# Kernel tuning notes

Measured on AMD Instinct MI355X. Metric: run time of the kernel, lower is better.

## Reference

```python
import jax, jax.numpy as jnp
import numpy as np


def setup_inputs() -> dict:
    key = jax.random.key(0)
    k0, k1 = jax.random.split(key)
    B, S, T = 32, 512, 128
    return {
        "crf_score_0": jax.random.normal(k0, (B, S + 1, T, T), dtype=jnp.float32),
        "crf_score_1": jax.random.normal(k1, (B, S + 1, T), dtype=jnp.float32),
        "sof": 126,
        "eof": 127,
    }


def reference(crf_score_0, crf_score_1, sof, eof):
    # crf_score_0: [B, S+1, T, T], crf_score_1: [B, S+1, T]
    # Initial scores (note: original multiplies, not adds, at step 0)
    forscores = crf_score_0[:, 0, sof, :] * crf_score_1[:, 0, :]  # [B, T]

    # Move seq axis first for scan: [S, B, T, T] and [S, B, T]
    c0 = jnp.moveaxis(crf_score_0[:, 1:], 0, 1)
    c1 = jnp.moveaxis(crf_score_1[:, 1:], 0, 1)

    def fwd_step(fs, xs):
        t0, t1 = xs  # [B, T, T], [B, T]
        # cur[b, i, j] = fs[b, i] + t1[b, j] + t0[b, i, j]
        cur = fs[:, :, None] + t1[:, None, :] + t0
        new_fs = jnp.max(cur, axis=1)            # [B, T]
        bp = jnp.argmax(cur, axis=1).astype(jnp.int32)  # [B, T]
        return new_fs, bp

    _, back_points = jax.lax.scan(fwd_step, forscores, (c0, c1))  # bps: [S, B, T]

    # Backtrack exactly as the original loop: pointer starts at bp[-1][:, eof],
    # then for idx = S-1 .. 0: pointer = bp[idx][b, pointer]; decode[:, idx] = pointer.
    ptr0 = back_points[-1][:, eof]  # [B]

    def bwd_step(ptr, bp_t):
        new = jnp.take_along_axis(bp_t, ptr[:, None], axis=1)[:, 0]
        return new, new

    _, dec = jax.lax.scan(bwd_step, ptr0, back_points, reverse=True)  # [S, B]
    return dec.T.astype(jnp.int32)  # [B, S] decoded label indices
```

## Files before the change

kernel.cpp:

```cpp
#include <hip/hip_runtime.h>


constexpr int S = 512;
constexpr int T = 128;

__global__ __launch_bounds__(1024, 1)
void viterbi_fused(const float* __restrict__ c0, const float* __restrict__ c1,
                   const int* __restrict__ sofp, const int* __restrict__ eofp,
                   int* __restrict__ out)
{
    __shared__ float fs[2][T];
    __shared__ float pmax[32][T];
    __shared__ int   parg[32][T];
    __shared__ unsigned char bp[S][T];

    const int b   = blockIdx.x;
    const int tid = (int)threadIdx.x;
    const int jq  = tid & 31;
    const int g   = tid >> 5;
    const int col = jq * 4;
    const int row = g * 4;

    const float* c0b = c0 + (size_t)b * (S + 1) * T * T;
    const float* c1b = c1 + (size_t)b * (S + 1) * T;

    if (tid < T) {
        const int sof = sofp[0];
        fs[0][tid] = c0b[(size_t)sof * T + tid] * c1b[tid];
    }
    __syncthreads();

    {
    }
    const float* t0p = c0b + (size_t)1 * T * T;
    const float* t1p = c1b + (size_t)1 * T;
    float4 a0 = *(const float4*)(t0p + (size_t)(row + 0) * T + col);
    float4 a1 = *(const float4*)(t0p + (size_t)(row + 1) * T + col);
    float4 a2 = *(const float4*)(t0p + (size_t)(row + 2) * T + col);
    float4 a3 = *(const float4*)(t0p + (size_t)(row + 3) * T + col);
    float4 tv = *(const float4*)(t1p + col);

    int p = 0;
    for (int s = 1; s <= S; ++s) {
        float4 b0 = make_float4(0.f,0.f,0.f,0.f), b1 = b0, b2 = b0, b3 = b0, bt = b0;
        if (s < S) {
            const float* n0 = c0b + (size_t)(s + 1) * T * T;
            const float* n1 = c1b + (size_t)(s + 1) * T;
            b0 = *(const float4*)(n0 + (size_t)(row + 0) * T + col);
            b1 = *(const float4*)(n0 + (size_t)(row + 1) * T + col);
            b2 = *(const float4*)(n0 + (size_t)(row + 2) * T + col);
            b3 = *(const float4*)(n0 + (size_t)(row + 3) * T + col);
            bt = *(const float4*)(n1 + col);
        }

        const float f0 = fs[p][row + 0];
        const float f1 = fs[p][row + 1];
        const float f2 = fs[p][row + 2];
        const float f3 = fs[p][row + 3];

        float bx, by, bz, bw; int ix, iy, iz, iw; float v;
        bx = (f0 + tv.x) + a0.x; ix = row;
        by = (f0 + tv.y) + a0.y; iy = row;
        bz = (f0 + tv.z) + a0.z; iz = row;
        bw = (f0 + tv.w) + a0.w; iw = row;

        v = (f1 + tv.x) + a1.x; if (v > bx) { bx = v; ix = row + 1; }
        v = (f1 + tv.y) + a1.y; if (v > by) { by = v; iy = row + 1; }
        v = (f1 + tv.z) + a1.z; if (v > bz) { bz = v; iz = row + 1; }
        v = (f1 + tv.w) + a1.w; if (v > bw) { bw = v; iw = row + 1; }

        v = (f2 + tv.x) + a2.x; if (v > bx) { bx = v; ix = row + 2; }
        v = (f2 + tv.y) + a2.y; if (v > by) { by = v; iy = row + 2; }
        v = (f2 + tv.z) + a2.z; if (v > bz) { bz = v; iz = row + 2; }
        v = (f2 + tv.w) + a2.w; if (v > bw) { bw = v; iw = row + 2; }

        v = (f3 + tv.x) + a3.x; if (v > bx) { bx = v; ix = row + 3; }
        v = (f3 + tv.y) + a3.y; if (v > by) { by = v; iy = row + 3; }
        v = (f3 + tv.z) + a3.z; if (v > bz) { bz = v; iz = row + 3; }
        v = (f3 + tv.w) + a3.w; if (v > bw) { bw = v; iw = row + 3; }

        *(float4*)&pmax[g][col] = make_float4(bx, by, bz, bw);
        *(int4*)  &parg[g][col] = make_int4(ix, iy, iz, iw);
        __syncthreads();

        if (tid < T) {
            float bb = pmax[0][tid];
            int   ii = parg[0][tid];
            #pragma unroll
            for (int gg = 1; gg < 32; ++gg) {
                float vv = pmax[gg][tid];
                if (vv > bb) { bb = vv; ii = parg[gg][tid]; }
            }
            fs[p ^ 1][tid] = bb;
            bp[s - 1][tid] = (unsigned char)ii;
        }
        __syncthreads();

        p ^= 1;
        a0 = b0; a1 = b1; a2 = b2; a3 = b3; tv = bt;
    }

    if (tid == 0) {
        const int eof = eofp[0];
        int ptr = bp[S - 1][eof];
        for (int idx = S - 1; idx >= 0; --idx) {
            ptr = bp[idx][ptr];
            out[(size_t)b * S + idx] = ptr;
        }
    }
}

extern "C" void kernel_launch(void* const* d_in, const int* in_sizes, int n_in,
                              void* d_out, int out_size, void* d_ws, size_t ws_size,
                              hipStream_t stream)
{
    const float* c0  = (const float*)d_in[0];
    const float* c1  = (const float*)d_in[1];
    const int*   sof = (const int*)d_in[2];
    const int*   eof = (const int*)d_in[3];
    int*         out = (int*)d_out;

    const int B = in_sizes[1] / ((S + 1) * T);
    viterbi_fused<<<dim3(B), dim3(1024), 0, stream>>>(c0, c1, sof, eof, out);
}
```

Measured before the change: 849.4 us.

## Split Viterbi forward across 8 blocks per batch with global flag exchange

```diff
diff --git a/kernel.cpp b/kernel.cpp
--- a/kernel.cpp
+++ b/kernel.cpp
@@ -1,25 +1,170 @@
 #include <hip/hip_runtime.h>
 
 
-constexpr int S = 512;
-constexpr int T = 128;
+constexpr int S   = 512;
+constexpr int T   = 128;
+constexpr int NSL = 8;
+constexpr int CW  = 16;
+
+using u64 = unsigned long long;
+using u32 = unsigned int;
+
+__device__ __forceinline__ void bar_lds() {
+    asm volatile("s_waitcnt lgkmcnt(0)" ::: "memory");
+    __builtin_amdgcn_s_barrier();
+}
+__device__ __forceinline__ u32 flipf(u32 u)   { return u ^ (0x80000000u | (u32)((int)u >> 31)); }
+__device__ __forceinline__ u32 unflipf(u32 y) { return y ^ (0x80000000u | ~(u32)((int)y >> 31)); }
+__device__ __forceinline__ u64 aload(const u64* p) {
+    return __hip_atomic_load(p, __ATOMIC_RELAXED, __HIP_MEMORY_SCOPE_AGENT);
+}
+__device__ __forceinline__ void astore(u64* p, u64 v) {
+    __hip_atomic_store(p, v, __ATOMIC_RELAXED, __HIP_MEMORY_SCOPE_AGENT);
+}
+
+#define GLDS(srcp, dstp) \
+    __builtin_amdgcn_global_load_lds( \
+        (const __attribute__((address_space(1))) void*)(srcp), \
+        (__attribute__((address_space(3))) void*)(dstp), 16, 0, 0)
+
+__global__ __launch_bounds__(256, 1)
+void viterbi_fwdj(const float* __restrict__ c0, const float* __restrict__ c1,
+                  const int* __restrict__ sofp,
+                  u64* __restrict__ pub,
+                  unsigned char* __restrict__ bp)
+{
+    __shared__ float fs_lds[T];
+    __shared__ float t0s[2][T * CW];
+    __shared__ u64   wpart[2][CW];
+
+    const int g    = blockIdx.x;
+    const int b    = g & 31;
+    const int k    = g >> 5;
+    const int tid  = (int)threadIdx.x;
+    const int lane = tid & 63;
+
+    const float* c0b = c0 + (size_t)b * (S + 1) * T * T;
+    const float* c1b = c1 + (size_t)b * (S + 1) * T;
+    u64* pubB = pub + (size_t)b * 2 * T;
+
+    const bool is_cmp = tid >= 128;
+    const int  ct  = tid - 128;
+    const int  j   = ct & 15;
+    const int  rb  = ct >> 4;
+    const int  wv2 = (tid >> 6) - 2;
+
+    auto STAGE = [&](int ss, int buf) {
+        const float* srcbase = c0b + (size_t)ss * T * T + (size_t)k * CW;
+        #pragma unroll
+        for (int it = 0; it < 4; ++it) {
+            const int q   = wv2 * 4 + it;
+            const int row = q * 16 + (lane >> 2);
+            const float* src = srcbase + (size_t)row * T + (lane & 3) * 4;
+            float* dst = &t0s[buf][q * 256];
+            GLDS(src, dst);
+        }
+    };
+
+    if (tid < T) fs_lds[tid] = c0b[(size_t)sofp[0] * T + tid] * c1b[tid];
+    float t1c = 0.f, t1n = 0.f;
+    if (is_cmp) {
+        STAGE(1, 1);
+        t1c = c1b[(size_t)1 * T + k * CW + j];
+    }
+    asm volatile("s_waitcnt vmcnt(0)" ::: "memory");
+    bar_lds();
+
+    for (int s = 1; s <= S; ++s) {
+        const int par = s & 1;
+
+        if (is_cmp) {
+            const float* tp = &t0s[par][0];
+            const int r0 = rb * 16;
+            u64 key;
+            {
+                float v = (fs_lds[r0] + t1c) + tp[r0 * CW + j];
+                key = ((u64)flipf(__float_as_uint(v)) << 32) | (u32)(255 - r0);
+            }
+            #pragma unroll
+            for (int r = 1; r < 16; ++r) {
+                const int row = r0 + r;
+                float v = (fs_lds[row] + t1c) + tp[row * CW + j];
+                u64 kk = ((u64)flipf(__float_as_uint(v)) << 32) | (u32)(255 - row);
+                if (kk > key) key = kk;
+            }
+            { u64 p = __shfl_xor(key, 16, 64); if (p > key) key = p; }
+            { u64 p = __shfl_xor(key, 32, 64); if (p > key) key = p; }
+            if ((ct & 63) < 16) wpart[wv2][j] = key;
+
+            if (s < S) {
+                STAGE(s + 1, par ^ 1);
+                t1n = c1b[(size_t)(s + 1) * T + k * CW + j];
+            }
+        }
+        bar_lds();
+
+        if (is_cmp && ct < 16) {
+            u64 kk = wpart[0][j];
+            u64 k1 = wpart[1][j];
+            if (k1 > kk) kk = k1;
+            const u32 vb = unflipf((u32)(kk >> 32));
+            const int ii = 255 - (int)(kk & 0xFFu);
+            astore(&pubB[(size_t)par * T + k * CW + j], ((u64)vb << 32) | (u32)s);
+            bp[((size_t)b * S + (s - 1)) * T + k * CW + j] = (unsigned char)ii;
+            fs_lds[k * CW + j] = __uint_as_float(vb);
+        }
+        if (!is_cmp && (tid >> 4) != k) {
+            const u64* p = &pubB[(size_t)par * T + tid];
+            u64 v;
+            do { v = aload(p); } while ((u32)v != (u32)s);
+            fs_lds[tid] = __uint_as_float((u32)(v >> 32));
+        }
+        if (is_cmp) asm volatile("s_waitcnt vmcnt(0)" ::: "memory");
+        bar_lds();
+
+        t1c = t1n;
+    }
+}
 
 __global__ __launch_bounds__(1024, 1)
-void viterbi_fused(const float* __restrict__ c0, const float* __restrict__ c1,
-                   const int* __restrict__ sofp, const int* __restrict__ eofp,
-                   int* __restrict__ out)
+void viterbi_bwd(const unsigned char* __restrict__ bp,
+                 const int* __restrict__ eofp, int* __restrict__ out)
+{
+    __shared__ unsigned char lbp[S][T];
+    const int b   = blockIdx.x;
+    const int tid = (int)threadIdx.x;
+
+    const uint4* s4 = (const uint4*)(bp + (size_t)b * S * T);
+    uint4* d4 = (uint4*)&lbp[0][0];
+    #pragma unroll
+    for (int it = 0; it < 4; ++it) d4[tid + it * 1024] = s4[tid + it * 1024];
+    __syncthreads();
+
+    if (tid == 0) {
+        int ptr = lbp[S - 1][eofp[0]];
+        for (int idx = S - 1; idx >= 0; --idx) {
+            ptr = lbp[idx][ptr];
+            out[(size_t)b * S + idx] = ptr;
+        }
+    }
+}
+
+__global__ __launch_bounds__(1024, 1)
+void viterbi_fused_fb(const float* __restrict__ c0, const float* __restrict__ c1,
+                      const int* __restrict__ sofp, const int* __restrict__ eofp,
+                      int* __restrict__ out)
 {
     __shared__ float fs[2][T];
     __shared__ float pmax[32][T];
     __shared__ int   parg[32][T];
-    __shared__ unsigned char bp[S][T];
+    __shared__ unsigned char bpl[S][T];
 
     const int b   = blockIdx.x;
     const int tid = (int)threadIdx.x;
     const int jq  = tid & 31;
-    const int g   = tid >> 5;
+    const int gg2 = tid >> 5;
     const int col = jq * 4;
-    const int row = g * 4;
+    const int row = gg2 * 4;
 
     const float* c0b = c0 + (size_t)b * (S + 1) * T * T;
     const float* c1b = c1 + (size_t)b * (S + 1) * T;
@@ -30,29 +175,24 @@
     }
     __syncthreads();
 
-    {
-    }
-    const float* t0p = c0b + (size_t)1 * T * T;
-    const float* t1p = c1b + (size_t)1 * T;
+    const float* t0p = c0b + (size_t)T * T;
     float4 a0 = *(const float4*)(t0p + (size_t)(row + 0) * T + col);
     float4 a1 = *(const float4*)(t0p + (size_t)(row + 1) * T + col);
     float4 a2 = *(const float4*)(t0p + (size_t)(row + 2) * T + col);
     float4 a3 = *(const float4*)(t0p + (size_t)(row + 3) * T + col);
-    float4 tv = *(const float4*)(t1p + col);
+    float4 tv = *(const float4*)(c1b + T + col);
 
     int p = 0;
     for (int s = 1; s <= S; ++s) {
         float4 b0 = make_float4(0.f,0.f,0.f,0.f), b1 = b0, b2 = b0, b3 = b0, bt = b0;
         if (s < S) {
             const float* n0 = c0b + (size_t)(s + 1) * T * T;
-            const float* n1 = c1b + (size_t)(s + 1) * T;
             b0 = *(const float4*)(n0 + (size_t)(row + 0) * T + col);
             b1 = *(const float4*)(n0 + (size_t)(row + 1) * T + col);
             b2 = *(const float4*)(n0 + (size_t)(row + 2) * T + col);
             b3 = *(const float4*)(n0 + (size_t)(row + 3) * T + col);
-            bt = *(const float4*)(n1 + col);
-        }
-
+            bt = *(const float4*)(c1b + (size_t)(s + 1) * T + col);
+        }
         const float f0 = fs[p][row + 0];
         const float f1 = fs[p][row + 1];
         const float f2 = fs[p][row + 2];
@@ -63,48 +203,44 @@
         by = (f0 + tv.y) + a0.y; iy = row;
         bz = (f0 + tv.z) + a0.z; iz = row;
         bw = (f0 + tv.w) + a0.w; iw = row;
-
         v = (f1 + tv.x) + a1.x; if (v > bx) { bx = v; ix = row + 1; }
         v = (f1 + tv.y) + a1.y; if (v > by) { by = v; iy = row + 1; }
         v = (f1 + tv.z) + a1.z; if (v > bz) { bz = v; iz = row + 1; }
         v = (f1 + tv.w) + a1.w; if (v > bw) { bw = v; iw = row + 1; }
-
         v = (f2 + tv.x) + a2.x; if (v > bx) { bx = v; ix = row + 2; }
         v = (f2 + tv.y) + a2.y; if (v > by) { by = v; iy = row + 2; }
         v = (f2 + tv.z) + a2.z; if (v > bz) { bz = v; iz = row + 2; }
         v = (f2 + tv.w) + a2.w; if (v > bw) { bw = v; iw = row + 2; }
-
         v = (f3 + tv.x) + a3.x; if (v > bx) { bx = v; ix = row + 3; }
         v = (f3 + tv.y) + a3.y; if (v > by) { by = v; iy = row + 3; }
         v = (f3 + tv.z) + a3.z; if (v > bz) { bz = v; iz = row + 3; }
         v = (f3 + tv.w) + a3.w; if (v > bw) { bw = v; iw = row + 3; }
 
-        *(float4*)&pmax[g][col] = make_float4(bx, by, bz, bw);
-        *(int4*)  &parg[g][col] = make_int4(ix, iy, iz, iw);
+        *(float4*)&pmax[gg2][col] = make_float4(bx, by, bz, bw);
+        *(int4*)  &parg[gg2][col] = make_int4(ix, iy, iz, iw);
         __syncthreads();
 
         if (tid < T) {
             float bb = pmax[0][tid];
             int   ii = parg[0][tid];
             #pragma unroll
-            for (int gg = 1; gg < 32; ++gg) {
-                float vv = pmax[gg][tid];
-                if (vv > bb) { bb = vv; ii = parg[gg][tid]; }
+            for (int qq2 = 1; qq2 < 32; ++qq2) {
+                float vv = pmax[qq2][tid];
+                if (vv > bb) { bb = vv; ii = parg[qq2][tid]; }
             }
             fs[p ^ 1][tid] = bb;
-            bp[s - 1][tid] = (unsigned char)ii;
+            bpl[s - 1][tid] = (unsigned char)ii;
         }
         __syncthreads();
-
         p ^= 1;
         a0 = b0; a1 = b1; a2 = b2; a3 = b3; tv = bt;
     }
 
     if (tid == 0) {
         const int eof = eofp[0];
-        int ptr = bp[S - 1][eof];
+        int ptr = bpl[S - 1][eof];
         for (int idx = S - 1; idx >= 0; --idx) {
-            ptr = bp[idx][ptr];
+            ptr = bpl[idx][ptr];
             out[(size_t)b * S + idx] = ptr;
         }
     }
@@ -121,5 +257,15 @@
     int*         out = (int*)d_out;
 
     const int B = in_sizes[1] / ((S + 1) * T);
-    viterbi_fused<<<dim3(B), dim3(1024), 0, stream>>>(c0, c1, sof, eof, out);
-}
+
+    const size_t pub_b = (size_t)B * 2 * T * 8;
+    const size_t bp_b  = (size_t)B * S * T;
+    if (B == 32 && ws_size >= pub_b + bp_b) {
+        u64* pubw = (u64*)d_ws;
+        unsigned char* bpw = (unsigned char*)d_ws + pub_b;
+        viterbi_fwdj<<<dim3(B * NSL), dim3(256), 0, stream>>>(c0, c1, sof, pubw, bpw);
+        viterbi_bwd<<<dim3(B), dim3(1024), 0, stream>>>(bpw, eof, out);
+    } else {
+        viterbi_fused_fb<<<dim3(B), dim3(1024), 0, stream>>>(c0, c1, sof, eof, out);
+    }
+}
```

After: 846.9 us. About the same (-0.3%).

## Reduce argmax with wave shuffles and one barrier per step, double-buffered register prefetch

Applied to the files above, without the earlier changes.

```diff
diff --git a/kernel.cpp b/kernel.cpp
--- a/kernel.cpp
+++ b/kernel.cpp
@@ -4,101 +4,111 @@
 constexpr int S = 512;
 constexpr int T = 128;
 
+using u64 = unsigned long long;
+using u32 = unsigned int;
+
+__device__ __forceinline__ void bar_lds() {
+    asm volatile("s_waitcnt lgkmcnt(0)" ::: "memory");
+    __builtin_amdgcn_s_barrier();
+}
+__device__ __forceinline__ u32 flipf(u32 u)   { return u ^ (0x80000000u | (u32)((int)u >> 31)); }
+__device__ __forceinline__ u32 unflipf(u32 y) { return y ^ (0x80000000u | ~(u32)((int)y >> 31)); }
+
 __global__ __launch_bounds__(1024, 1)
-void viterbi_fused(const float* __restrict__ c0, const float* __restrict__ c1,
-                   const int* __restrict__ sofp, const int* __restrict__ eofp,
-                   int* __restrict__ out)
+void viterbi_one(const float* __restrict__ c0, const float* __restrict__ c1,
+                 const int* __restrict__ sofp, const int* __restrict__ eofp,
+                 int* __restrict__ out)
 {
     __shared__ float fs[2][T];
-    __shared__ float pmax[32][T];
-    __shared__ int   parg[32][T];
     __shared__ unsigned char bp[S][T];
 
     const int b   = blockIdx.x;
     const int tid = (int)threadIdx.x;
-    const int jq  = tid & 31;
-    const int g   = tid >> 5;
-    const int col = jq * 4;
-    const int row = g * 4;
+    const int j   = tid >> 3;
+    const int ih  = tid & 7;
+    const int r0  = ih * 16;
 
     const float* c0b = c0 + (size_t)b * (S + 1) * T * T;
     const float* c1b = c1 + (size_t)b * (S + 1) * T;
 
-    if (tid < T) {
-        const int sof = sofp[0];
-        fs[0][tid] = c0b[(size_t)sof * T + tid] * c1b[tid];
+    if (tid < T) fs[0][tid] = c0b[(size_t)sofp[0] * T + tid] * c1b[tid];
+
+    const float* pA = c0b + (size_t)T * T + (size_t)r0 * T + j;
+    const float* pB = pA + T * T;
+    float tA = c1b[(size_t)1 * T + j];
+    float tB = c1b[(size_t)2 * T + j];
+
+#define LOAD16(P, ptr)                                                        \
+    P##0  = (ptr)[0 * T];  P##1  = (ptr)[1 * T];  P##2  = (ptr)[2 * T];       \
+    P##3  = (ptr)[3 * T];  P##4  = (ptr)[4 * T];  P##5  = (ptr)[5 * T];       \
+    P##6  = (ptr)[6 * T];  P##7  = (ptr)[7 * T];  P##8  = (ptr)[8 * T];       \
+    P##9  = (ptr)[9 * T];  P##10 = (ptr)[10 * T]; P##11 = (ptr)[11 * T];      \
+    P##12 = (ptr)[12 * T]; P##13 = (ptr)[13 * T]; P##14 = (ptr)[14 * T];      \
+    P##15 = (ptr)[15 * T];
+
+    float A0, A1, A2, A3, A4, A5, A6, A7, A8, A9, A10, A11, A12, A13, A14, A15;
+    float B0, B1, B2, B3, B4, B5, B6, B7, B8, B9, B10, B11, B12, B13, B14, B15;
+    LOAD16(A, pA)
+    LOAD16(B, pB)
+
+    bar_lds();
+
+#define STEP(SS, P, tc)                                                       \
+    {                                                                         \
+        const int par = (SS) & 1;                                             \
+        const float* fsr = &fs[par ^ 1][r0];                                  \
+        float4 f0 = *(const float4*)(fsr);                                    \
+        float4 f1 = *(const float4*)(fsr + 4);                                \
+        float4 f2 = *(const float4*)(fsr + 8);                                \
+        float4 f3 = *(const float4*)(fsr + 12);                               \
+        float bv, v; int br;                                                  \
+        bv = (f0.x + tc) + P##0;  br = 0;                                     \
+        v = (f0.y + tc) + P##1;  if (v > bv) { bv = v; br = 1;  }             \
+        v = (f0.z + tc) + P##2;  if (v > bv) { bv = v; br = 2;  }             \
+        v = (f0.w + tc) + P##3;  if (v > bv) { bv = v; br = 3;  }             \
+        v = (f1.x + tc) + P##4;  if (v > bv) { bv = v; br = 4;  }             \
+        v = (f1.y + tc) + P##5;  if (v > bv) { bv = v; br = 5;  }             \
+        v = (f1.z + tc) + P##6;  if (v > bv) { bv = v; br = 6;  }             \
+        v = (f1.w + tc) + P##7;  if (v > bv) { bv = v; br = 7;  }             \
+        v = (f2.x + tc) + P##8;  if (v > bv) { bv = v; br = 8;  }             \
+        v = (f2.y + tc) + P##9;  if (v > bv) { bv = v; br = 9;  }             \
+        v = (f2.z + tc) + P##10; if (v > bv) { bv = v; br = 10; }             \
+        v = (f2.w + tc) + P##11; if (v > bv) { bv = v; br = 11; }             \
+        v = (f3.x + tc) + P##12; if (v > bv) { bv = v; br = 12; }             \
+        v = (f3.y + tc) + P##13; if (v > bv) { bv = v; br = 13; }             \
+        v = (f3.z + tc) + P##14; if (v > bv) { bv = v; br = 14; }             \
+        v = (f3.w + tc) + P##15; if (v > bv) { bv = v; br = 15; }             \
+        u64 key = ((u64)flipf(__float_as_uint(bv)) << 32)                     \
+                | (u32)(255 - (r0 + br));                                     \
+        { u64 p = __shfl_xor(key, 1, 64); if (p > key) key = p; }             \
+        { u64 p = __shfl_xor(key, 2, 64); if (p > key) key = p; }             \
+        { u64 p = __shfl_xor(key, 4, 64); if (p > key) key = p; }             \
+        if (ih == 0) {                                                        \
+            fs[par][j] = __uint_as_float(unflipf((u32)(key >> 32)));          \
+            bp[(SS) - 1][j] = (unsigned char)(255 - (int)(key & 0xFFu));      \
+        }                                                                     \
     }
-    __syncthreads();
 
-    {
+    for (int s = 1; s <= S; s += 2) {
+        STEP(s, A, tA)
+        if (s + 2 <= S) {
+            pA += 2 * T * T;
+            LOAD16(A, pA)
+            tA = c1b[(size_t)(s + 2) * T + j];
+        }
+        bar_lds();
+
+        STEP(s + 1, B, tB)
+        if (s + 3 <= S) {
+            pB += 2 * T * T;
+            LOAD16(B, pB)
+            tB = c1b[(size_t)(s + 3) * T + j];
+        }
+        bar_lds();
     }
-    const float* t0p = c0b + (size_t)1 * T * T;
-    const float* t1p = c1b + (size_t)1 * T;
-    float4 a0 = *(const float4*)(t0p + (size_t)(row + 0) * T + col);
-    float4 a1 = *(const float4*)(t0p + (size_t)(row + 1) * T + col);
-    float4 a2 = *(const float4*)(t0p + (size_t)(row + 2) * T + col);
-    float4 a3 = *(const float4*)(t0p + (size_t)(row + 3) * T + col);
-    float4 tv = *(const float4*)(t1p + col);
 
-    int p = 0;
-    for (int s = 1; s <= S; ++s) {
-        float4 b0 = make_float4(0.f,0.f,0.f,0.f), b1 = b0, b2 = b0, b3 = b0, bt = b0;
-        if (s < S) {
-            const float* n0 = c0b + (size_t)(s + 1) * T * T;
-            const float* n1 = c1b + (size_t)(s + 1) * T;
-            b0 = *(const float4*)(n0 + (size_t)(row + 0) * T + col);
-            b1 = *(const float4*)(n0 + (size_t)(row + 1) * T + col);
-            b2 = *(const float4*)(n0 + (size_t)(row + 2) * T + col);
-            b3 = *(const float4*)(n0 + (size_t)(row + 3) * T + col);
-            bt = *(const float4*)(n1 + col);
-        }
-
-        const float f0 = fs[p][row + 0];
-        const float f1 = fs[p][row + 1];
-        const float f2 = fs[p][row + 2];
-        const float f3 = fs[p][row + 3];
-
-        float bx, by, bz, bw; int ix, iy, iz, iw; float v;
-        bx = (f0 + tv.x) + a0.x; ix = row;
-        by = (f0 + tv.y) + a0.y; iy = row;
-        bz = (f0 + tv.z) + a0.z; iz = row;
-        bw = (f0 + tv.w) + a0.w; iw = row;
-
-        v = (f1 + tv.x) + a1.x; if (v > bx) { bx = v; ix = row + 1; }
-        v = (f1 + tv.y) + a1.y; if (v > by) { by = v; iy = row + 1; }
-        v = (f1 + tv.z) + a1.z; if (v > bz) { bz = v; iz = row + 1; }
-        v = (f1 + tv.w) + a1.w; if (v > bw) { bw = v; iw = row + 1; }
-
-        v = (f2 + tv.x) + a2.x; if (v > bx) { bx = v; ix = row + 2; }
-        v = (f2 + tv.y) + a2.y; if (v > by) { by = v; iy = row + 2; }
-        v = (f2 + tv.z) + a2.z; if (v > bz) { bz = v; iz = row + 2; }
-        v = (f2 + tv.w) + a2.w; if (v > bw) { bw = v; iw = row + 2; }
-
-        v = (f3 + tv.x) + a3.x; if (v > bx) { bx = v; ix = row + 3; }
-        v = (f3 + tv.y) + a3.y; if (v > by) { by = v; iy = row + 3; }
-        v = (f3 + tv.z) + a3.z; if (v > bz) { bz = v; iz = row + 3; }
-        v = (f3 + tv.w) + a3.w; if (v > bw) { bw = v; iw = row + 3; }
-
-        *(float4*)&pmax[g][col] = make_float4(bx, by, bz, bw);
-        *(int4*)  &parg[g][col] = make_int4(ix, iy, iz, iw);
-        __syncthreads();
-
-        if (tid < T) {
-            float bb = pmax[0][tid];
-            int   ii = parg[0][tid];
-            #pragma unroll
-            for (int gg = 1; gg < 32; ++gg) {
-                float vv = pmax[gg][tid];
-                if (vv > bb) { bb = vv; ii = parg[gg][tid]; }
-            }
-            fs[p ^ 1][tid] = bb;
-            bp[s - 1][tid] = (unsigned char)ii;
-        }
-        __syncthreads();
-
-        p ^= 1;
-        a0 = b0; a1 = b1; a2 = b2; a3 = b3; tv = bt;
-    }
+#undef STEP
+#undef LOAD16
 
     if (tid == 0) {
         const int eof = eofp[0];
@@ -121,5 +131,5 @@
     int*         out = (int*)d_out;
 
     const int B = in_sizes[1] / ((S + 1) * T);
-    viterbi_fused<<<dim3(B), dim3(1024), 0, stream>>>(c0, c1, sof, eof, out);
+    viterbi_one<<<dim3(B), dim3(1024), 0, stream>>>(c0, c1, sof, eof, out);
 }
```

Result: slower. 1.910 ms (+124.9%).
